# Performance work log

Measured on AMD Instinct MI355X. Metric: run time of the kernel, lower is better.

Reference implementation:

```python
import jax, jax.numpy as jnp
import numpy as np

D_MODEL = 1472
N_HEADS = 6
D_KV = 64
INNER = N_HEADS * D_KV
NUM_BUCKETS = 32
MAX_DIST = 128


def _relative_position_bucket(relative_position, bidirectional=True,
                              num_buckets=NUM_BUCKETS, max_distance=MAX_DIST):
    ret = jnp.zeros_like(relative_position)
    if bidirectional:
        num_buckets //= 2
        ret = ret + (relative_position > 0).astype(jnp.int32) * num_buckets
        rel = jnp.abs(relative_position)
    else:
        rel = -jnp.minimum(relative_position, 0)
    max_exact = num_buckets // 2
    is_small = rel < max_exact
    rel_f = jnp.maximum(rel, 1).astype(jnp.float32)
    large = max_exact + (
        jnp.log(rel_f / max_exact) / np.log(max_distance / max_exact)
        * (num_buckets - max_exact)
    ).astype(jnp.int32)
    large = jnp.minimum(large, num_buckets - 1)
    return ret + jnp.where(is_small, rel, large)


def _position_bias(q_len, k_len, rel_bias):
    # rel_bias: [num_buckets, n_heads]
    ctx = jnp.arange(q_len)[:, None]
    mem = jnp.arange(k_len)[None, :]
    buckets = _relative_position_bucket(mem - ctx, bidirectional=True)
    values = rel_bias[buckets]                 # [Q, K, H]
    return jnp.transpose(values, (2, 0, 1))[None]  # [1, H, Q, K]


def setup_inputs() -> dict:
    key = jax.random.key(0)
    ks = jax.random.split(key, 8)
    B, S = 4, 2048
    scale = 0.02
    return {
        "kv_sequences": jax.random.normal(ks[0], (B, S, D_MODEL), jnp.float32),
        "q_sequences": jax.random.normal(ks[1], (B, S, D_MODEL), jnp.float32),
        "mask": jnp.zeros((B, 1, S, S), jnp.float32),
        "WQ": jax.random.normal(ks[2], (D_MODEL, INNER), jnp.float32) * scale,
        "WK": jax.random.normal(ks[3], (D_MODEL, INNER), jnp.float32) * scale,
        "WV": jax.random.normal(ks[4], (D_MODEL, INNER), jnp.float32) * scale,
        "WO": jax.random.normal(ks[5], (INNER, D_MODEL), jnp.float32) * scale,
        "rel_bias": jax.random.normal(ks[6], (NUM_BUCKETS, N_HEADS), jnp.float32) * scale,
    }


def reference(kv_sequences, q_sequences, mask, WQ, WK, WV, WO, rel_bias):
    B, Kl, _ = kv_sequences.shape
    Ql = q_sequences.shape[1]
    # projections -> [B, H, L, d_kv]
    q = (q_sequences @ WQ).reshape(B, Ql, N_HEADS, D_KV).transpose(0, 2, 1, 3)
    k = (kv_sequences @ WK).reshape(B, Kl, N_HEADS, D_KV).transpose(0, 2, 1, 3)
    v = (kv_sequences @ WV).reshape(B, Kl, N_HEADS, D_KV).transpose(0, 2, 1, 3)
    # T5-style: no 1/sqrt(d) scaling
    logits = jnp.einsum("bhqd,bhkd->bhqk", q, k)
    logits = logits + _position_bias(Ql, Kl, rel_bias)
    logits = logits + mask
    attn = jax.nn.softmax(logits.astype(jnp.float32), axis=-1).astype(logits.dtype)
    out = jnp.einsum("bhqk,bhkd->bhqd", attn, v)
    out = out.transpose(0, 2, 1, 3).reshape(B, Ql, INNER)
    return out @ WO
```

## Files before the change

kernel.cpp:

```cpp
#include <hip/hip_runtime.h>
#include <hip/hip_fp16.h>
#include <cstdint>

#define DM    1472
#define NH    6
#define DKV   64
#define INNER 384
#define BATCH 4
#define SEQ   2048
#define LOG2E 1.4426950408889634f

typedef __attribute__((ext_vector_type(8))) _Float16 half8;
typedef __attribute__((ext_vector_type(4))) _Float16 half4;
typedef __attribute__((ext_vector_type(4))) float f32x4;

__device__ __forceinline__ void gload16(const void* g, const void* l) {
  __builtin_amdgcn_global_load_lds((const __attribute__((address_space(1))) void*)g,
                                   (__attribute__((address_space(3))) void*)l, 16, 0, 0);
}

__global__ void prep_weights(const float* __restrict__ WQ, const float* __restrict__ WK,
                             const float* __restrict__ WV, const float* __restrict__ WO,
                             _Float16* __restrict__ WqT, _Float16* __restrict__ WkT,
                             _Float16* __restrict__ WvT, _Float16* __restrict__ WoT) {
  int idx = blockIdx.x * blockDim.x + threadIdx.x;
  const int per = DM * INNER;
  if (idx >= 4 * per) return;
  int which = idx / per;
  int i = idx - which * per;
  if (which < 3) {
    const float* W = which == 0 ? WQ : (which == 1 ? WK : WV);
    _Float16* T = which == 0 ? WqT : (which == 1 ? WkT : WvT);
    int k = i / INNER, n = i - (i / INNER) * INNER;
    T[(size_t)n * DM + k] = (_Float16)W[i];
  } else {
    int k = i / DM, n = i - (i / DM) * DM;
    WoT[(size_t)n * INNER + k] = (_Float16)WO[i];
  }
}

__global__ void prep_bias(const float* __restrict__ rel_bias, float* __restrict__ biasS) {
  int idx = blockIdx.x * blockDim.x + threadIdx.x;
  const int TOT = NH * 4 * 4104;
  if (idx >= TOT) return;
  int h = idx / (4 * 4104);
  int rem = idx - h * 4 * 4104;
  int cc = rem / 4104;
  int i = rem - cc * 4104;
  int j = i + cc; if (j > 4094) j = 4094;
  int d = j - 2047;
  int ret = d > 0 ? 16 : 0;
  int a = d < 0 ? -d : d;
  int bucket;
  if (a < 8) bucket = ret + a;
  else {
    int large;
    if      (a >= 91) large = 15;
    else if (a >= 64) large = 14;
    else if (a >= 46) large = 13;
    else if (a >= 32) large = 12;
    else if (a >= 23) large = 11;
    else if (a >= 16) large = 10;
    else if (a >= 12) large = 9;
    else              large = 8;
    bucket = ret + large;
  }
  biasS[idx] = rel_bias[bucket * NH + h] * LOG2E;
}

__global__ __launch_bounds__(256) void prep_maskflags(const float* __restrict__ mask,
                                                      int* __restrict__ flags) {
  const int bid = blockIdx.x;
  const int kh = bid & 1;
  const int qt = (bid >> 1) & 31;
  const int b = bid >> 6;
  const int tid = threadIdx.x;
  __shared__ int fl[16];
  if (tid < 16) fl[tid] = 0;
  __syncthreads();
  const float* base = mask + ((size_t)(b * SEQ + qt * 64)) * SEQ + kh * 1024 + tid * 4;
  bool nz = false;
  for (int q = 0; q < 64; ++q) {
    f32x4 v = *(const f32x4*)(base + (size_t)q * SEQ);
    nz |= (v[0] != 0.f) | (v[1] != 0.f) | (v[2] != 0.f) | (v[3] != 0.f);
  }
  if (nz) fl[tid >> 4] = 1;
  __syncthreads();
  if (tid < 16) flags[(size_t)b * 1024 + qt * 32 + kh * 16 + tid] = fl[tid];
}

__global__ __launch_bounds__(256) void proj_gemm(
    const float* __restrict__ Xq, const float* __restrict__ Xkv,
    const _Float16* __restrict__ WqT, const _Float16* __restrict__ WkvT,
    _Float16* __restrict__ Qo, _Float16* __restrict__ Ko, _Float16* __restrict__ Vto) {
  const int bm = blockIdx.x, by = blockIdx.y;
  const bool isQ = by < 3;
  const float* __restrict__ X = isQ ? Xq : Xkv;
  const _Float16* __restrict__ WT = isQ ? (WqT + (size_t)by * 128 * DM)
                                        : (WkvT + (size_t)(by - 3) * 128 * DM);

  __shared__ alignas(16) float    As[2][128 * 32];
  __shared__ alignas(16) _Float16 Bs[2][128 * 32];

  const int tid = threadIdx.x;
  const int lane = tid & 63, wave = tid >> 6;
  const int wm = wave >> 1, wn = wave & 1;
  const int l15 = lane & 15, lg = lane >> 4;

  f32x4 acc[4][4] = {};

  const int aoff = 4 * ((lane & 7) ^ (lane >> 3));
  const float* asrc[4];
#pragma unroll
  for (int c = 0; c < 4; ++c)
    asrc[c] = X + (size_t)(bm * 128 + (wave * 4 + c) * 8 + (lane >> 3)) * DM + aoff;
  const int boff = 8 * ((lane & 3) ^ ((lane >> 3) & 3));
  const _Float16* bsrc[2];
#pragma unroll
  for (int c = 0; c < 2; ++c)
    bsrc[c] = WT + (size_t)((wave * 2 + c) * 16 + (lane >> 2)) * DM + boff;

  const int NT = DM / 32;

#pragma unroll
  for (int c = 0; c < 4; ++c)
    gload16(asrc[c], (const char*)&As[0][0] + (wave * 4 + c) * 1024);
#pragma unroll
  for (int c = 0; c < 2; ++c)
    gload16(bsrc[c], (const char*)&Bs[0][0] + (wave * 2 + c) * 1024);
#pragma unroll
  for (int c = 0; c < 4; ++c)
    gload16(asrc[c] + 32, (const char*)&As[1][0] + (wave * 4 + c) * 1024);
#pragma unroll
  for (int c = 0; c < 2; ++c)
    gload16(bsrc[c] + 32, (const char*)&Bs[1][0] + (wave * 2 + c) * 1024);

  for (int t = 0; t < NT; ++t) {
    if (t + 1 < NT) asm volatile("s_waitcnt vmcnt(6)" ::: "memory");
    else            asm volatile("s_waitcnt vmcnt(0)" ::: "memory");
    __builtin_amdgcn_s_barrier();
    __builtin_amdgcn_sched_barrier(0);

    const char* Ab = (const char*)&As[t & 1][0];
    const char* Bb = (const char*)&Bs[t & 1][0];
    half8 af[4], bf[4];
#pragma unroll
    for (int m = 0; m < 4; ++m) {
      int r = wm * 64 + m * 16 + l15;
      int s = (r & 7) << 4;
      f32x4 x0 = *(const f32x4*)(Ab + r * 128 + ((lg * 32) ^ s));
      f32x4 x1 = *(const f32x4*)(Ab + r * 128 + ((lg * 32 + 16) ^ s));
      half8 h;
#pragma unroll
      for (int j = 0; j < 4; ++j) { h[j] = (_Float16)x0[j]; h[4 + j] = (_Float16)x1[j]; }
      af[m] = h;
    }
#pragma unroll
    for (int n = 0; n < 4; ++n) {
      int r = wn * 64 + n * 16 + l15;
      bf[n] = *(const half8*)(Bb + r * 64 + ((lg * 16) ^ (((r >> 1) & 3) << 4)));
    }

    __builtin_amdgcn_s_setprio(1);
#pragma unroll
    for (int m = 0; m < 4; ++m)
#pragma unroll
      for (int n = 0; n < 4; ++n)
        acc[m][n] = __builtin_amdgcn_mfma_f32_16x16x32_f16(af[m], bf[n], acc[m][n], 0, 0, 0);
    __builtin_amdgcn_s_setprio(0);

    __builtin_amdgcn_sched_barrier(0);
    __builtin_amdgcn_s_barrier();
    if (t + 2 < NT) {
      const int kf = (t + 2) * 32;
#pragma unroll
      for (int c = 0; c < 4; ++c)
        gload16(asrc[c] + kf, (const char*)&As[t & 1][0] + (wave * 4 + c) * 1024);
#pragma unroll
      for (int c = 0; c < 2; ++c)
        gload16(bsrc[c] + kf, (const char*)&Bs[t & 1][0] + (wave * 2 + c) * 1024);
    }
  }

#pragma unroll
  for (int m = 0; m < 4; ++m)
#pragma unroll
    for (int n = 0; n < 4; ++n)
#pragma unroll
      for (int r = 0; r < 4; ++r) {
        int gm = bm * 128 + wm * 64 + m * 16 + lg * 4 + r;
        int gnl = wn * 64 + n * 16 + l15;
        int b = gm >> 11, s = gm & 2047;
        float av = acc[m][n][r];
        if (isQ) {
          int gn = by * 128 + gnl;
          int h = gn >> 6, dd = gn & 63;
          Qo[((size_t)(b * NH + h) * SEQ + s) * DKV + dd] = (_Float16)(av * LOG2E);
        } else {
          int gn = (by - 3) * 128 + gnl;
          if (gn < INNER) {
            int h = gn >> 6, dd = gn & 63;
            Ko[((size_t)(b * NH + h) * SEQ + s) * DKV + dd] = (_Float16)av;
          } else {
            int gnv = gn - INNER;
            int h = gnv >> 6, dd = gnv & 63;
            Vto[((size_t)(b * NH + h) * DKV + dd) * SEQ + s] = (_Float16)av;
          }
        }
      }
}

__global__ __launch_bounds__(256, 4) void attn_kernel(
    const _Float16* __restrict__ Q, const _Float16* __restrict__ K, const _Float16* __restrict__ Vt,
    const float* __restrict__ biasS, const float* __restrict__ mask,
    const int* __restrict__ mflags, _Float16* __restrict__ AO) {
  const int bid = blockIdx.x;
  const int g = (bid & 7) * 96 + (bid >> 3);
  const int bh = g >> 5, qb = g & 31;
  const int b = bh / NH, h = bh - b * NH;
  const int q0 = qb * 64;
  const int NT = SEQ / 64;

  const int tid = threadIdx.x, lane = tid & 63, wave = tid >> 6;
  const int l15 = lane & 15, lg = lane >> 4;

  __shared__ alignas(16) _Float16 Ks[2][64 * 64];
  __shared__ alignas(16) _Float16 Vs[2][64 * 64];
  __shared__ alignas(16) _Float16 Ps[4][16 * 64];

  const size_t bhS = (size_t)bh * SEQ;
  const int qq = q0 + wave * 16 + l15;

  const _Float16* Qbase = Q + (bhS + q0 + wave * 16) * DKV;
  half8 qf0 = *(const half8*)(Qbase + (size_t)l15 * DKV + lg * 8);
  half8 qf1 = *(const half8*)(Qbase + (size_t)l15 * DKV + 32 + lg * 8);

  const float* maskrow = mask + (size_t)b * SEQ * SEQ + (size_t)qq * SEQ + lg * 4;
  const int c = (3 - l15) & 3;
  const float* bbase = biasS + (size_t)(h * 4 + c) * 4104 + (lg * 4 - qq + 2047 - c);
  const int* mfl = mflags + b * 1024 + qb * 32;

  float m_r = -1e30f, l_acc = 0.f;
  f32x4 oacc[4] = {};

  const int rl = lane >> 3;
  const int sw = ((lane & 7) ^ rl) * 8;
  const _Float16* Kd0 = K + (bhS + wave * 16 + rl) * DKV + sw;
  const _Float16* Kd1 = Kd0 + 8 * DKV;
  const _Float16* Vd0 = Vt + ((size_t)bh * DKV + wave * 16 + rl) * SEQ + sw;
  const _Float16* Vd1 = Vd0 + 8 * SEQ;
  char* KsB = (char*)&Ks[0][0];
  char* VsB = (char*)&Vs[0][0];
  char* PsB = (char*)&Ps[wave][0];
  const int dmaLds = wave * 2048;

  gload16(Kd0, KsB + dmaLds);
  gload16(Kd1, KsB + dmaLds + 1024);
  gload16(Vd0, VsB + dmaLds);
  gload16(Vd1, VsB + dmaLds + 1024);
  gload16(Kd0 + 64 * DKV, KsB + 8192 + dmaLds);
  gload16(Kd1 + 64 * DKV, KsB + 8192 + dmaLds + 1024);
  gload16(Vd0 + 64, VsB + 8192 + dmaLds);
  gload16(Vd1 + 64, VsB + 8192 + dmaLds + 1024);

  for (int t = 0; t < NT; ++t) {
    if (t + 1 < NT) asm volatile("s_waitcnt vmcnt(4)" ::: "memory");
    else            asm volatile("s_waitcnt vmcnt(0)" ::: "memory");
    __builtin_amdgcn_s_barrier();
    __builtin_amdgcn_sched_barrier(0);

    const int mflag = mfl[t];
    const char* Kb = KsB + (t & 1) * 8192;
    const char* Vb = VsB + (t & 1) * 8192;

    f32x4 sacc[4] = {};
    __builtin_amdgcn_s_setprio(1);
#pragma unroll
    for (int nf = 0; nf < 4; ++nf) {
      int kr = nf * 16 + l15;
      const char* rb = Kb + kr * 128;
      half8 kf0 = *(const half8*)(rb + ((lg ^ (kr & 7)) << 4));
      half8 kf1 = *(const half8*)(rb + (((4 + lg) ^ (kr & 7)) << 4));
      sacc[nf] = __builtin_amdgcn_mfma_f32_16x16x32_f16(kf0, qf0, sacc[nf], 0, 0, 0);
      sacc[nf] = __builtin_amdgcn_mfma_f32_16x16x32_f16(kf1, qf1, sacc[nf], 0, 0, 0);
    }
    __builtin_amdgcn_s_setprio(0);

    float sv[4][4], fm[4];
#pragma unroll
    for (int nf = 0; nf < 4; ++nf) {
      f32x4 bv = *(const f32x4*)(bbase + t * 64 + nf * 16);
#pragma unroll
      for (int r = 0; r < 4; ++r)
        sv[nf][r] = sacc[nf][r] + bv[r];
    }
    if (mflag) {
#pragma unroll
      for (int nf = 0; nf < 4; ++nf) {
        f32x4 mv = *(const f32x4*)(maskrow + t * 64 + nf * 16);
#pragma unroll
        for (int r = 0; r < 4; ++r)
          sv[nf][r] += mv[r] * LOG2E;
      }
    }
#pragma unroll
    for (int nf = 0; nf < 4; ++nf)
      fm[nf] = fmaxf(fmaxf(sv[nf][0], sv[nf][1]), fmaxf(sv[nf][2], sv[nf][3]));
    float mx = fmaxf(fmaxf(fm[0], fm[1]), fmaxf(fm[2], fm[3]));
    mx = fmaxf(mx, __shfl_xor(mx, 16));
    mx = fmaxf(mx, __shfl_xor(mx, 32));

    if (!__all(mx <= m_r + 8.0f)) {
      float mnew = fmaxf(m_r, mx);
      float sc_ = __builtin_amdgcn_exp2f(m_r - mnew);
      m_r = mnew;
      l_acc *= sc_;
      f32x4 scv;
#pragma unroll
      for (int r = 0; r < 4; ++r) scv[r] = __shfl(sc_, lg * 4 + r);
#pragma unroll
      for (int df = 0; df < 4; ++df) oacc[df] *= scv;
    }

    float rs = 0.f;
#pragma unroll
    for (int nf = 0; nf < 4; ++nf) {
      half4 ph;
#pragma unroll
      for (int r = 0; r < 4; ++r) {
        float p = __builtin_amdgcn_exp2f(sv[nf][r] - m_r);
        rs += p;
        ph[r] = (_Float16)p;
      }
      *(half4*)(PsB + l15 * 128 + ((((nf << 1) + (lg >> 1)) ^ (l15 & 7)) << 4) + ((lg & 1) << 3)) = ph;
    }
    l_acc += rs;

    __builtin_amdgcn_s_setprio(1);
#pragma unroll
    for (int ks = 0; ks < 2; ++ks) {
      half8 pa = *(const half8*)(PsB + l15 * 128 + ((((ks << 2) + lg) ^ (l15 & 7)) << 4));
#pragma unroll
      for (int df = 0; df < 4; ++df) {
        int vr = df * 16 + l15;
        half8 vv = *(const half8*)(Vb + vr * 128 + ((((ks << 2) + lg) ^ (vr & 7)) << 4));
        oacc[df] = __builtin_amdgcn_mfma_f32_16x16x32_f16(pa, vv, oacc[df], 0, 0, 0);
      }
    }
    __builtin_amdgcn_s_setprio(0);

    __builtin_amdgcn_sched_barrier(0);
    __builtin_amdgcn_s_barrier();
    if (t + 2 < NT) {
      char* kb = KsB + (t & 1) * 8192 + dmaLds;
      char* vb_ = VsB + (t & 1) * 8192 + dmaLds;
      gload16(Kd0 + (size_t)(t + 2) * 64 * DKV, kb);
      gload16(Kd1 + (size_t)(t + 2) * 64 * DKV, kb + 1024);
      gload16(Vd0 + (t + 2) * 64, vb_);
      gload16(Vd1 + (t + 2) * 64, vb_ + 1024);
    }
  }

  l_acc += __shfl_xor(l_acc, 16);
  l_acc += __shfl_xor(l_acc, 32);
  f32x4 lv;
#pragma unroll
  for (int r = 0; r < 4; ++r) lv[r] = __shfl(l_acc, lg * 4 + r);
#pragma unroll
  for (int df = 0; df < 4; ++df) {
    int dd = df * 16 + l15;
#pragma unroll
    for (int r = 0; r < 4; ++r) {
      int qrow = q0 + wave * 16 + lg * 4 + r;
      AO[((size_t)(b * SEQ + qrow)) * INNER + h * DKV + dd] = (_Float16)(oacc[df][r] / lv[r]);
    }
  }
}

__global__ __launch_bounds__(256) void out_gemm(
    const _Float16* __restrict__ A, const _Float16* __restrict__ BT, float* __restrict__ C) {
  __shared__ alignas(16) _Float16 As[2][128 * 32];
  __shared__ alignas(16) _Float16 Bs[2][64 * 32];

  const int tid = threadIdx.x, lane = tid & 63, wave = tid >> 6;
  const int wm = wave >> 1, wn = wave & 1;
  const int bm = blockIdx.x, bn = blockIdx.y;
  const int l15 = lane & 15, lg = lane >> 4;

  f32x4 acc[4][2] = {};

  const int rl4 = (lane >> 2) & 3;
  const int soff = ((lane & 3) ^ rl4) * 8;
  const _Float16* ad0 = A + (size_t)(bm * 128 + (wave * 2) * 16 + (lane >> 2)) * INNER + soff;
  const _Float16* ad1 = ad0 + (size_t)16 * INNER;
  const _Float16* bd0 = BT + (size_t)(bn * 64 + wave * 16 + (lane >> 2)) * INNER + soff;
  char* AsB = (char*)&As[0][0];
  char* BsB = (char*)&Bs[0][0];
  const int aLds = wave * 2048;
  const int bLds = wave * 1024;

  const int NT = INNER / 32;

  gload16(ad0, AsB + aLds);
  gload16(ad1, AsB + aLds + 1024);
  gload16(bd0, BsB + bLds);
  __syncthreads();

  for (int t = 0; t < NT; ++t) {
    if (t + 1 < NT) {
      const int nb = (t + 1) & 1;
      const int kf = (t + 1) * 32;
      gload16(ad0 + kf, AsB + nb * 8192 + aLds);
      gload16(ad1 + kf, AsB + nb * 8192 + aLds + 1024);
      gload16(bd0 + kf, BsB + nb * 4096 + bLds);
    }

    const char* Ab = AsB + (t & 1) * 8192;
    const char* Bb = BsB + (t & 1) * 4096;
    half8 af[4], bf[2];
#pragma unroll
    for (int m = 0; m < 4; ++m) {
      int r = wm * 64 + m * 16 + l15;
      af[m] = *(const half8*)(Ab + r * 64 + (((lg ^ (r & 3))) << 4));
    }
#pragma unroll
    for (int n = 0; n < 2; ++n) {
      int r = wn * 32 + n * 16 + l15;
      bf[n] = *(const half8*)(Bb + r * 64 + (((lg ^ (r & 3))) << 4));
    }
    __builtin_amdgcn_s_setprio(1);
#pragma unroll
    for (int m = 0; m < 4; ++m)
#pragma unroll
      for (int n = 0; n < 2; ++n)
        acc[m][n] = __builtin_amdgcn_mfma_f32_16x16x32_f16(af[m], bf[n], acc[m][n], 0, 0, 0);
    __builtin_amdgcn_s_setprio(0);

    __syncthreads();
  }

#pragma unroll
  for (int m = 0; m < 4; ++m)
#pragma unroll
    for (int n = 0; n < 2; ++n)
#pragma unroll
      for (int r = 0; r < 4; ++r) {
        int gm = bm * 128 + wm * 64 + m * 16 + lg * 4 + r;
        int gn = bn * 64 + wn * 32 + n * 16 + l15;
        C[(size_t)gm * DM + gn] = acc[m][n][r];
      }
}

extern "C" void kernel_launch(void* const* d_in, const int* in_sizes, int n_in,
                              void* d_out, int out_size, void* d_ws, size_t ws_size,
                              hipStream_t stream) {
  const float* kv   = (const float*)d_in[0];
  const float* qs   = (const float*)d_in[1];
  const float* mask = (const float*)d_in[2];
  const float* WQ   = (const float*)d_in[3];
  const float* WK   = (const float*)d_in[4];
  const float* WV   = (const float*)d_in[5];
  const float* WO   = (const float*)d_in[6];
  const float* rb   = (const float*)d_in[7];
  float* out = (float*)d_out;
  char* ws = (char*)d_ws;

  const size_t WT_BYTES  = (size_t)INNER * DM * 2;
  const size_t QKV_BYTES = (size_t)BATCH * NH * SEQ * DKV * 2;
  _Float16* WqT = (_Float16*)(ws);
  _Float16* WkT = (_Float16*)(ws + WT_BYTES);
  _Float16* WvT = (_Float16*)(ws + 2 * WT_BYTES);
  _Float16* WoT = (_Float16*)(ws + 3 * WT_BYTES);
  _Float16* Qh  = (_Float16*)(ws + 4 * WT_BYTES);
  _Float16* Kh  = (_Float16*)(ws + 4 * WT_BYTES + QKV_BYTES);
  _Float16* Vth = (_Float16*)(ws + 4 * WT_BYTES + 2 * QKV_BYTES);
  _Float16* AO  = (_Float16*)(ws + 4 * WT_BYTES + 3 * QKV_BYTES);
  float* biasS  = (float*)(ws + 4 * WT_BYTES + 4 * QKV_BYTES);
  int* mflags   = (int*)(ws + 4 * WT_BYTES + 4 * QKV_BYTES + (size_t)NH * 4 * 4104 * 4);

  hipLaunchKernelGGL(prep_weights, dim3((4 * DM * INNER + 255) / 256), dim3(256), 0, stream,
                     WQ, WK, WV, WO, WqT, WkT, WvT, WoT);
  hipLaunchKernelGGL(prep_bias, dim3((NH * 4 * 4104 + 255) / 256), dim3(256), 0, stream, rb, biasS);
  hipLaunchKernelGGL(prep_maskflags, dim3(BATCH * 32 * 2), dim3(256), 0, stream, mask, mflags);
  hipLaunchKernelGGL(proj_gemm, dim3(64, 9), dim3(256), 0, stream,
                     qs, kv, WqT, WkT, Qh, Kh, Vth);
  hipLaunchKernelGGL(attn_kernel, dim3(768), dim3(256), 0, stream,
                     Qh, Kh, Vth, biasS, mask, mflags, AO);
  hipLaunchKernelGGL(out_gemm, dim3(64, 23), dim3(256), 0, stream, AO, WoT, out);
}
```

Before: 178.1 us.

## Widen projection GEMM tile to 128x384 with 512-thread blocks

The projection GEMM now uses 8 waves per block and a 128x384 output tile, so each block covers a whole Q, K or V projection. This is meant to load and convert each fp32 X tile once per projection instead of three times, cutting global traffic. The cost is a grid of only 192 blocks, fewer than twice the CU count, plus more accumulator registers per wave (96 floats) and more LDS per block, which may leave CUs idle and limit latency hiding.

```diff
diff --git a/kernel.cpp b/kernel.cpp
--- a/kernel.cpp
+++ b/kernel.cpp
@@ -89,61 +89,59 @@
   if (tid < 16) flags[(size_t)b * 1024 + qt * 32 + kh * 16 + tid] = fl[tid];
 }
 
-__global__ __launch_bounds__(256) void proj_gemm(
+__global__ __launch_bounds__(512, 2) void proj_gemm(
     const float* __restrict__ Xq, const float* __restrict__ Xkv,
     const _Float16* __restrict__ WqT, const _Float16* __restrict__ WkvT,
     _Float16* __restrict__ Qo, _Float16* __restrict__ Ko, _Float16* __restrict__ Vto) {
   const int bm = blockIdx.x, by = blockIdx.y;
-  const bool isQ = by < 3;
-  const float* __restrict__ X = isQ ? Xq : Xkv;
-  const _Float16* __restrict__ WT = isQ ? (WqT + (size_t)by * 128 * DM)
-                                        : (WkvT + (size_t)(by - 3) * 128 * DM);
+  const float* __restrict__ X = (by == 0) ? Xq : Xkv;
+  const _Float16* __restrict__ WT = (by == 0) ? WqT : (WkvT + (size_t)(by - 1) * 384 * DM);
 
   __shared__ alignas(16) float    As[2][128 * 32];
-  __shared__ alignas(16) _Float16 Bs[2][128 * 32];
+  __shared__ alignas(16) _Float16 Bs[2][384 * 32];
 
   const int tid = threadIdx.x;
   const int lane = tid & 63, wave = tid >> 6;
-  const int wm = wave >> 1, wn = wave & 1;
+  const int wm = wave >> 2, wn = wave & 3;
   const int l15 = lane & 15, lg = lane >> 4;
 
-  f32x4 acc[4][4] = {};
+  f32x4 acc[4][6] = {};
 
   const int aoff = 4 * ((lane & 7) ^ (lane >> 3));
-  const float* asrc[4];
-#pragma unroll
-  for (int c = 0; c < 4; ++c)
-    asrc[c] = X + (size_t)(bm * 128 + (wave * 4 + c) * 8 + (lane >> 3)) * DM + aoff;
+  const float* asrc[2];
+#pragma unroll
+  for (int c = 0; c < 2; ++c)
+    asrc[c] = X + (size_t)(bm * 128 + (wave * 2 + c) * 8 + (lane >> 3)) * DM + aoff;
   const int boff = 8 * ((lane & 3) ^ ((lane >> 3) & 3));
-  const _Float16* bsrc[2];
+  const _Float16* bsrc[3];
+#pragma unroll
+  for (int c = 0; c < 3; ++c)
+    bsrc[c] = WT + (size_t)((wave * 3 + c) * 16 + (lane >> 2)) * DM + boff;
+
+  const int NT = DM / 32;
+
 #pragma unroll
   for (int c = 0; c < 2; ++c)
-    bsrc[c] = WT + (size_t)((wave * 2 + c) * 16 + (lane >> 2)) * DM + boff;
-
-  const int NT = DM / 32;
-
-#pragma unroll
-  for (int c = 0; c < 4; ++c)
-    gload16(asrc[c], (const char*)&As[0][0] + (wave * 4 + c) * 1024);
+    gload16(asrc[c], (const char*)&As[0][0] + (wave * 2 + c) * 1024);
+#pragma unroll
+  for (int c = 0; c < 3; ++c)
+    gload16(bsrc[c], (const char*)&Bs[0][0] + (wave * 3 + c) * 1024);
 #pragma unroll
   for (int c = 0; c < 2; ++c)
-    gload16(bsrc[c], (const char*)&Bs[0][0] + (wave * 2 + c) * 1024);
-#pragma unroll
-  for (int c = 0; c < 4; ++c)
-    gload16(asrc[c] + 32, (const char*)&As[1][0] + (wave * 4 + c) * 1024);
-#pragma unroll
-  for (int c = 0; c < 2; ++c)
-    gload16(bsrc[c] + 32, (const char*)&Bs[1][0] + (wave * 2 + c) * 1024);
+    gload16(asrc[c] + 32, (const char*)&As[1][0] + (wave * 2 + c) * 1024);
+#pragma unroll
+  for (int c = 0; c < 3; ++c)
+    gload16(bsrc[c] + 32, (const char*)&Bs[1][0] + (wave * 3 + c) * 1024);
 
   for (int t = 0; t < NT; ++t) {
-    if (t + 1 < NT) asm volatile("s_waitcnt vmcnt(6)" ::: "memory");
+    if (t + 1 < NT) asm volatile("s_waitcnt vmcnt(5)" ::: "memory");
     else            asm volatile("s_waitcnt vmcnt(0)" ::: "memory");
     __builtin_amdgcn_s_barrier();
     __builtin_amdgcn_sched_barrier(0);
 
     const char* Ab = (const char*)&As[t & 1][0];
     const char* Bb = (const char*)&Bs[t & 1][0];
-    half8 af[4], bf[4];
+    half8 af[4];
 #pragma unroll
     for (int m = 0; m < 4; ++m) {
       int r = wm * 64 + m * 16 + l15;
@@ -155,9 +153,10 @@
       for (int j = 0; j < 4; ++j) { h[j] = (_Float16)x0[j]; h[4 + j] = (_Float16)x1[j]; }
       af[m] = h;
     }
-#pragma unroll
-    for (int n = 0; n < 4; ++n) {
-      int r = wn * 64 + n * 16 + l15;
+    half8 bf[6];
+#pragma unroll
+    for (int n = 0; n < 6; ++n) {
+      int r = wn * 96 + n * 16 + l15;
       bf[n] = *(const half8*)(Bb + r * 64 + ((lg * 16) ^ (((r >> 1) & 3) << 4)));
     }
 
@@ -165,7 +164,7 @@
 #pragma unroll
     for (int m = 0; m < 4; ++m)
 #pragma unroll
-      for (int n = 0; n < 4; ++n)
+      for (int n = 0; n < 6; ++n)
         acc[m][n] = __builtin_amdgcn_mfma_f32_16x16x32_f16(af[m], bf[n], acc[m][n], 0, 0, 0);
     __builtin_amdgcn_s_setprio(0);
 
@@ -174,39 +173,28 @@
     if (t + 2 < NT) {
       const int kf = (t + 2) * 32;
 #pragma unroll
-      for (int c = 0; c < 4; ++c)
-        gload16(asrc[c] + kf, (const char*)&As[t & 1][0] + (wave * 4 + c) * 1024);
-#pragma unroll
       for (int c = 0; c < 2; ++c)
-        gload16(bsrc[c] + kf, (const char*)&Bs[t & 1][0] + (wave * 2 + c) * 1024);
+        gload16(asrc[c] + kf, (const char*)&As[t & 1][0] + (wave * 2 + c) * 1024);
+#pragma unroll
+      for (int c = 0; c < 3; ++c)
+        gload16(bsrc[c] + kf, (const char*)&Bs[t & 1][0] + (wave * 3 + c) * 1024);
     }
   }
 
 #pragma unroll
   for (int m = 0; m < 4; ++m)
 #pragma unroll
-    for (int n = 0; n < 4; ++n)
+    for (int n = 0; n < 6; ++n)
 #pragma unroll
       for (int r = 0; r < 4; ++r) {
         int gm = bm * 128 + wm * 64 + m * 16 + lg * 4 + r;
-        int gnl = wn * 64 + n * 16 + l15;
+        int gnl = wn * 96 + n * 16 + l15;
         int b = gm >> 11, s = gm & 2047;
+        int h = gnl >> 6, dd = gnl & 63;
         float av = acc[m][n][r];
-        if (isQ) {
-          int gn = by * 128 + gnl;
-          int h = gn >> 6, dd = gn & 63;
-          Qo[((size_t)(b * NH + h) * SEQ + s) * DKV + dd] = (_Float16)(av * LOG2E);
-        } else {
-          int gn = (by - 3) * 128 + gnl;
-          if (gn < INNER) {
-            int h = gn >> 6, dd = gn & 63;
-            Ko[((size_t)(b * NH + h) * SEQ + s) * DKV + dd] = (_Float16)av;
-          } else {
-            int gnv = gn - INNER;
-            int h = gnv >> 6, dd = gnv & 63;
-            Vto[((size_t)(b * NH + h) * DKV + dd) * SEQ + s] = (_Float16)av;
-          }
-        }
+        if (by == 0)      Qo[((size_t)(b * NH + h) * SEQ + s) * DKV + dd] = (_Float16)(av * LOG2E);
+        else if (by == 1) Ko[((size_t)(b * NH + h) * SEQ + s) * DKV + dd] = (_Float16)av;
+        else              Vto[((size_t)(b * NH + h) * DKV + dd) * SEQ + s] = (_Float16)av;
       }
 }
 
@@ -482,7 +470,7 @@
                      WQ, WK, WV, WO, WqT, WkT, WvT, WoT);
   hipLaunchKernelGGL(prep_bias, dim3((NH * 4 * 4104 + 255) / 256), dim3(256), 0, stream, rb, biasS);
   hipLaunchKernelGGL(prep_maskflags, dim3(BATCH * 32 * 2), dim3(256), 0, stream, mask, mflags);
-  hipLaunchKernelGGL(proj_gemm, dim3(64, 9), dim3(256), 0, stream,
+  hipLaunchKernelGGL(proj_gemm, dim3(64, 3), dim3(512), 0, stream,
                      qs, kv, WqT, WkT, Qh, Kh, Vth);
   hipLaunchKernelGGL(attn_kernel, dim3(768), dim3(256), 0, stream,
                      Qh, Kh, Vth, biasS, mask, mflags, AO);
```

Measured after the change: 202.9 us. 1.14x slower.
